# Kernel tuning notes

Measured on AMD Instinct MI355X. Metric: run time of the kernel, lower is better.

Reference implementation:

```python
import jax, jax.numpy as jnp
import numpy as np

N_NODES = 50000
N_EDGES = 800000
IN_CH = 3
HID = 32
OUT_CH = 16
HEADS = 8
NEG_SLOPE = 0.2  # PyG GATConv default LeakyReLU slope


def setup_inputs() -> dict:
    key = jax.random.key(0)
    ks = jax.random.split(key, 12)
    x = jax.random.normal(ks[0], (N_NODES, IN_CH), dtype=jnp.float32)
    edge_index = jax.random.randint(ks[1], (2, N_EDGES), 0, N_NODES, dtype=jnp.int64)
    # Layer 1: GATConv(3 -> 32, heads=8, concat=True)
    s1 = 1.0 / np.sqrt(IN_CH)
    W1 = jax.random.uniform(ks[2], (IN_CH, HEADS * HID), jnp.float32, -s1, s1)
    att_src1 = jax.random.uniform(ks[3], (HEADS, HID), jnp.float32, -s1, s1)
    att_dst1 = jax.random.uniform(ks[4], (HEADS, HID), jnp.float32, -s1, s1)
    bias1 = jnp.zeros((HEADS * HID,), jnp.float32)
    # Layer 2: GATConv(256 -> 16, heads=1, concat=False)
    s2 = 1.0 / np.sqrt(HEADS * HID)
    W2 = jax.random.uniform(ks[5], (HEADS * HID, 1 * OUT_CH), jnp.float32, -s2, s2)
    att_src2 = jax.random.uniform(ks[6], (1, OUT_CH), jnp.float32, -s2, s2)
    att_dst2 = jax.random.uniform(ks[7], (1, OUT_CH), jnp.float32, -s2, s2)
    bias2 = jnp.zeros((OUT_CH,), jnp.float32)
    return {"x": x, "edge_index": edge_index,
            "W1": W1, "att_src1": att_src1, "att_dst1": att_dst1, "bias1": bias1,
            "W2": W2, "att_src2": att_src2, "att_dst2": att_dst2, "bias2": bias2}


def gat_conv(x, src, dst, W, att_src, att_dst, bias, heads, out_ch, concat):
    """PyG-style GATConv (eval mode: attention dropout is identity).
    src/dst already include self-loops. Returns [N, heads*out_ch] or [N, out_ch]."""
    N = x.shape[0]
    h = (x @ W).reshape(N, heads, out_ch)                      # [N,H,C]
    a_s = jnp.einsum("nhc,hc->nh", h, att_src)                 # [N,H]
    a_d = jnp.einsum("nhc,hc->nh", h, att_dst)                 # [N,H]
    e = jax.nn.leaky_relu(a_s[src] + a_d[dst], NEG_SLOPE)      # [E,H]
    # segment softmax over incoming edges of each dst node
    m = jax.ops.segment_max(e, dst, num_segments=N)            # [N,H]
    e = jnp.exp(e - m[dst])
    denom = jax.ops.segment_sum(e, dst, num_segments=N)        # [N,H]
    alpha = e / (denom[dst] + 1e-16)                           # [E,H]
    msg = h[src] * alpha[:, :, None]                           # [E,H,C]
    out = jax.ops.segment_sum(msg, dst, num_segments=N)        # [N,H,C]
    out = out.reshape(N, heads * out_ch) if concat else out.mean(axis=1)
    return out + bias


def reference(x, edge_index, W1, att_src1, att_dst1, bias1, W2, att_src2, att_dst2, bias2):
    N = x.shape[0]
    loop = jnp.arange(N, dtype=edge_index.dtype)
    src = jnp.concatenate([edge_index[0], loop])  # add self-loops (PyG default)
    dst = jnp.concatenate([edge_index[1], loop])
    h = gat_conv(x, src, dst, W1, att_src1, att_dst1, bias1, HEADS, HID, True)
    h = jax.nn.elu(h)
    out = gat_conv(h, src, dst, W2, att_src2, att_dst2, bias2, 1, OUT_CH, False)
    return out
```

## Files before the change

kernel.cpp:

```cpp
#include <hip/hip_runtime.h>
#include <math.h>

#define N_NODES 50000
#define N_EDGES 800000
#define E_TOT   850000
#define HEADS   8
#define HID     32
#define C1      256
#define OUTC    16
#define NEG     0.2f
#define NBKT    196
#define BCAP    6144
#define EPB     2048
#define NSB     ((E_TOT + EPB - 1) / EPB)

__device__ __forceinline__ float lrelu(float v) { return v > 0.0f ? v : NEG * v; }

__device__ unsigned g_bcnt[256];

__global__ __launch_bounds__(256) void k_setup(
    const float* __restrict__ x, const int* __restrict__ ei,
    const float* __restrict__ W1,
    const float* __restrict__ att_s1, const float* __restrict__ att_d1,
    const float* __restrict__ W2,
    const float* __restrict__ att_s2, const float* __restrict__ att_d2,
    float4* __restrict__ xp, unsigned* __restrict__ ebuf,
    float* __restrict__ As1, float* __restrict__ Ad1,
    float* __restrict__ As2, float* __restrict__ Ad2)
{
    __shared__ unsigned hist[256];
    __shared__ unsigned gpos[256];
    int t = threadIdx.x;
    int blk = blockIdx.x;
    if (blk == 0) {
        if (t < 24) {
            int k = t / 8, h = t % 8;
            float as = 0.0f, ad = 0.0f;
            for (int c = 0; c < HID; c++) {
                float w = W1[k * C1 + h * HID + c];
                as = fmaf(w, att_s1[h * HID + c], as);
                ad = fmaf(w, att_d1[h * HID + c], ad);
            }
            As1[k * 8 + h] = as; Ad1[k * 8 + h] = ad;
        }
        float as2 = 0.0f, ad2 = 0.0f;
        for (int j = 0; j < OUTC; j++) {
            float w = W2[t * OUTC + j];
            as2 = fmaf(w, att_s2[j], as2);
            ad2 = fmaf(w, att_d2[j], ad2);
        }
        As2[t] = as2; Ad2[t] = ad2;
    }
    int nid = blk * 256 + t;
    if (nid < N_NODES)
        xp[nid] = make_float4(x[nid * 3], x[nid * 3 + 1], x[nid * 3 + 2], 1.0f);

    hist[t] = 0;
    __syncthreads();
    unsigned pk[8]; unsigned short rk[8]; unsigned char bk[8];
    int e0 = blk * EPB;
    #pragma unroll
    for (int j = 0; j < 8; j++) {
        int e = e0 + j * 256 + t;
        if (e < E_TOT) {
            int s, d;
            if (e < N_EDGES) { s = ei[e]; d = ei[N_EDGES + e]; }
            else             { s = d = e - N_EDGES; }
            pk[j] = ((unsigned)d << 16) | (unsigned)s;
            int b = d >> 8;
            bk[j] = (unsigned char)b;
            rk[j] = (unsigned short)atomicAdd(&hist[b], 1u);
        } else { pk[j] = 0u; bk[j] = 0; rk[j] = 0; }
    }
    __syncthreads();
    unsigned c = hist[t];
    gpos[t] = c ? atomicAdd(&g_bcnt[t], c) : 0u;
    __syncthreads();
    #pragma unroll
    for (int j = 0; j < 8; j++) {
        int e = e0 + j * 256 + t;
        if (e < E_TOT) {
            unsigned b = bk[j];
            ebuf[b * BCAP + gpos[b] + rk[j]] = pk[j];
        }
    }
}

__global__ __launch_bounds__(256) void k_csr(
    const unsigned* __restrict__ ebuf,
    int* __restrict__ off, unsigned short* __restrict__ csr)
{
    __shared__ unsigned s[256];
    __shared__ unsigned dcnt[256];
    __shared__ unsigned dscan[256];
    int t = threadIdx.x, b = blockIdx.x;
    unsigned cntb = g_bcnt[b];
    s[t] = (t < NBKT) ? g_bcnt[t] : 0u;
    dcnt[t] = 0u;
    __syncthreads();
    for (int o = 1; o < 256; o <<= 1) {
        unsigned v = (t >= o) ? s[t - o] : 0u;
        __syncthreads();
        s[t] += v;
        __syncthreads();
    }
    unsigned base = (b == 0) ? 0u : s[b - 1];
    unsigned ev[24]; unsigned short rk[24];
    #pragma unroll
    for (int j = 0; j < 24; j++) {
        int i = j * 256 + t;
        if (i < (int)cntb) {
            unsigned v = ebuf[b * BCAP + i];
            ev[j] = v;
            rk[j] = (unsigned short)atomicAdd(&dcnt[(v >> 16) & 255u], 1u);
        } else { ev[j] = 0u; rk[j] = 0; }
    }
    __syncthreads();
    dscan[t] = dcnt[t];
    __syncthreads();
    for (int o = 1; o < 256; o <<= 1) {
        unsigned v = (t >= o) ? dscan[t - o] : 0u;
        __syncthreads();
        dscan[t] += v;
        __syncthreads();
    }
    int d = b * 256 + t;
    if (d <= N_NODES) off[d] = (int)(base + dscan[t] - dcnt[t]);
    #pragma unroll
    for (int j = 0; j < 24; j++) {
        int i = j * 256 + t;
        if (i < (int)cntb) {
            unsigned d8 = (ev[j] >> 16) & 255u;
            unsigned pos = base + (dscan[d8] - dcnt[d8]) + rk[j];
            csr[pos] = (unsigned short)(ev[j] & 0xFFFFu);
        }
    }
}

__global__ __launch_bounds__(256) void k_agg1(
    const int* __restrict__ off, const unsigned short* __restrict__ csr,
    const float4* __restrict__ xp,
    const float* __restrict__ As1, const float* __restrict__ Ad1,
    float4* __restrict__ xaccw)
{
    int tid = threadIdx.x;
    if (blockIdx.x == 0) g_bcnt[tid] = 0;
    int h = tid & 7;
    int dst = blockIdx.x * 32 + (tid >> 3);
    if (dst >= N_NODES) return;
    float s0 = As1[h], s1 = As1[8 + h], s2 = As1[16 + h];
    float d0 = Ad1[h], d1 = Ad1[8 + h], d2 = Ad1[16 + h];
    float4 xd = xp[dst];
    float ad = xd.x * d0 + xd.y * d1 + xd.z * d2;
    int beg = off[dst], end = off[dst + 1];
    float a0 = 0.0f, a1 = 0.0f, a2 = 0.0f, a3 = 0.0f;
    int k = beg;
    for (; k + 8 <= end; k += 8) {
        int sm[8]; float4 xv[8];
        #pragma unroll
        for (int j = 0; j < 8; j++) sm[j] = csr[k + j];
        #pragma unroll
        for (int j = 0; j < 8; j++) xv[j] = xp[sm[j]];
        #pragma unroll
        for (int j = 0; j < 8; j++) {
            float as = xv[j].x * s0 + xv[j].y * s1 + xv[j].z * s2;
            float p = __expf(lrelu(as + ad));
            a0 = fmaf(p, xv[j].x, a0);
            a1 = fmaf(p, xv[j].y, a1);
            a2 = fmaf(p, xv[j].z, a2);
            a3 += p;
        }
    }
    if (k < end) {
        int m = end - k;
        int sm[8]; float4 xv[8];
        #pragma unroll
        for (int j = 0; j < 8; j++) { int idx = k + j; sm[j] = csr[idx < end ? idx : k]; }
        #pragma unroll
        for (int j = 0; j < 8; j++) xv[j] = xp[sm[j]];
        #pragma unroll
        for (int j = 0; j < 8; j++) {
            float as = xv[j].x * s0 + xv[j].y * s1 + xv[j].z * s2;
            float p = __expf(lrelu(as + ad));
            p = (j < m) ? p : 0.0f;
            a0 = fmaf(p, xv[j].x, a0);
            a1 = fmaf(p, xv[j].y, a1);
            a2 = fmaf(p, xv[j].z, a2);
            a3 += p;
        }
    }
    xaccw[dst * 8 + h] = make_float4(a0, a1, a2, a3);
}

__global__ __launch_bounds__(256) void k_fin1h2(
    const float4* __restrict__ xaccw, const float* __restrict__ W1,
    const float* __restrict__ b1, const float* __restrict__ W2,
    const float* __restrict__ As2, const float* __restrict__ Ad2,
    float* __restrict__ h2, float* __restrict__ a_s2, float* __restrict__ a_d2)
{
    __shared__ float sW1[3 * C1];
    __shared__ float sAux[3 * C1];
    __shared__ float sW2t[OUTC][260];
    __shared__ float sElu[16][260];
    int t = threadIdx.x;
    for (int i = t; i < 3 * C1; i += 256) sW1[i] = W1[i];
    sAux[t] = b1[t]; sAux[C1 + t] = As2[t]; sAux[2 * C1 + t] = Ad2[t];
    for (int i = t; i < C1 * OUTC; i += 256) {
        int k = i >> 4, j = i & 15;
        sW2t[j][k] = W2[i];
    }
    __syncthreads();
    int n = t >> 4, l = t & 15;
    int node = blockIdx.x * 16 + n;
    float as = 0.0f, ad = 0.0f;
    for (int i = 0; i < 16; i++) {
        int c = l + 16 * i;
        int h = c >> 5;
        float4 xa = xaccw[node * 8 + h];
        float z = (xa.x * sW1[c] + xa.y * sW1[C1 + c] + xa.z * sW1[2 * C1 + c])
                  / (xa.w + 1e-16f) + sAux[c];
        float e = z > 0.0f ? z : expm1f(z);
        sElu[n][c] = e;
        as = fmaf(e, sAux[C1 + c], as);
        ad = fmaf(e, sAux[2 * C1 + c], ad);
    }
    for (int o = 1; o < 16; o <<= 1) {
        as += __shfl_xor(as, o, 64);
        ad += __shfl_xor(ad, o, 64);
    }
    if (l == 0) { a_s2[node] = as; a_d2[node] = ad; }
    __syncthreads();
    const float4* e4 = (const float4*)&sElu[n][0];
    const float4* w4 = (const float4*)&sW2t[l][0];
    float acc = 0.0f;
    #pragma unroll 8
    for (int k = 0; k < 64; k++) {
        float4 a = e4[k], b = w4[k];
        acc = fmaf(a.x, b.x, fmaf(a.y, b.y, fmaf(a.z, b.z, fmaf(a.w, b.w, acc))));
    }
    h2[node * OUTC + l] = acc;
}

__global__ __launch_bounds__(256) void k_agg2(
    const int* __restrict__ off, const unsigned short* __restrict__ csr,
    const float* __restrict__ a_s, const float* __restrict__ a_d,
    const float* __restrict__ h2, const float* __restrict__ bias,
    float* __restrict__ out)
{
    int tid = threadIdx.x;
    int c = tid & 15;
    int dst = blockIdx.x * 16 + (tid >> 4);
    if (dst >= N_NODES) return;
    int beg = off[dst], end = off[dst + 1];
    float ad = a_d[dst];
    float acc = 0.0f, denp = 0.0f;
    int k = beg;
    for (; k + 8 <= end; k += 8) {
        int sm[8]; float p[8];
        #pragma unroll
        for (int j = 0; j < 8; j++) sm[j] = csr[k + j];
        #pragma unroll
        for (int j = 0; j < 8; j++) p[j] = __expf(lrelu(a_s[sm[j]] + ad));
        #pragma unroll
        for (int j = 0; j < 8; j++) {
            denp += p[j];
            acc = fmaf(p[j], h2[sm[j] * OUTC + c], acc);
        }
    }
    if (k < end) {
        int m = end - k;
        int sm[8]; float p[8];
        #pragma unroll
        for (int j = 0; j < 8; j++) { int idx = k + j; sm[j] = csr[idx < end ? idx : k]; }
        #pragma unroll
        for (int j = 0; j < 8; j++) {
            float pj = __expf(lrelu(a_s[sm[j]] + ad));
            p[j] = (j < m) ? pj : 0.0f;
        }
        #pragma unroll
        for (int j = 0; j < 8; j++) {
            denp += p[j];
            acc = fmaf(p[j], h2[sm[j] * OUTC + c], acc);
        }
    }
    out[dst * OUTC + c] = acc / (denp + 1e-16f) + bias[c];
}

extern "C" void kernel_launch(void* const* d_in, const int* in_sizes, int n_in,
                              void* d_out, int out_size, void* d_ws, size_t ws_size,
                              hipStream_t stream)
{
    (void)in_sizes; (void)n_in; (void)out_size; (void)ws_size;
    const float* x    = (const float*)d_in[0];
    const int*   ei   = (const int*)d_in[1];
    const float* W1   = (const float*)d_in[2];
    const float* as1w = (const float*)d_in[3];
    const float* ad1w = (const float*)d_in[4];
    const float* b1   = (const float*)d_in[5];
    const float* W2   = (const float*)d_in[6];
    const float* as2w = (const float*)d_in[7];
    const float* ad2w = (const float*)d_in[8];
    const float* b2   = (const float*)d_in[9];
    float* out = (float*)d_out;

    const long N = N_NODES;
    char* p = (char*)d_ws;
    auto alloc = [&](size_t elems) {
        void* r = p; p += ((elems + 3) & ~(size_t)3) * 4; return r;
    };

    float4*         xp     = (float4*)alloc(N * 4);
    float4*         xaccw  = (float4*)alloc(N * HEADS * 4);
    unsigned*       ebuf   = (unsigned*)alloc((size_t)NBKT * BCAP);
    int*            off    = (int*)alloc(N + 1);
    unsigned short* csr    = (unsigned short*)alloc((E_TOT + 1) / 2);
    float*          As1    = (float*)alloc(32);
    float*          Ad1    = (float*)alloc(32);
    float*          As2    = (float*)alloc(C1);
    float*          Ad2    = (float*)alloc(C1);
    float*          h2v    = (float*)alloc(N * OUTC);
    float*          a_s2   = (float*)alloc(N);
    float*          a_d2   = (float*)alloc(N);

    k_setup<<<NSB, 256, 0, stream>>>(
        x, ei, W1, as1w, ad1w, W2, as2w, ad2w,
        xp, ebuf, As1, Ad1, As2, Ad2);
    k_csr<<<NBKT, 256, 0, stream>>>(ebuf, off, csr);
    k_agg1<<<(int)((N + 31) / 32), 256, 0, stream>>>(off, csr, xp, As1, Ad1, xaccw);
    k_fin1h2<<<(int)(N / 16), 256, 0, stream>>>(xaccw, W1, b1, W2, As2, Ad2, h2v, a_s2, a_d2);
    k_agg2<<<(int)((N + 15) / 16), 256, 0, stream>>>(off, csr, a_s2, a_d2, h2v, b2, out);
}
```

Measured before the change: 165.1 us.

## Pre-gather source features into edge-ordered buffer during CSR build, widen CSR blocks

The CSR build kernel now also gathers each edge's source node features into a new edge-ordered float4 array, written at the same position as the CSR index. The layer-1 aggregation then reads these features contiguously instead of doing an index load followed by a random gather. The CSR kernel also goes from 256 to 512 threads per block. The cost is about 13.6 MB of extra scattered writes and reads of a per-edge feature array, in exchange for removing the dependent index-then-gather chain in the aggregation.

New measurement: 166.1 us. No clear change (+0.6%).

```diff
diff --git a/kernel.cpp b/kernel.cpp
--- a/kernel.cpp
+++ b/kernel.cpp
@@ -86,29 +86,29 @@
     }
 }
 
-__global__ __launch_bounds__(256) void k_csr(
-    const unsigned* __restrict__ ebuf,
-    int* __restrict__ off, unsigned short* __restrict__ csr)
+__global__ __launch_bounds__(512) void k_csr(
+    const unsigned* __restrict__ ebuf, const float4* __restrict__ xp,
+    int* __restrict__ off, unsigned short* __restrict__ csr,
+    float4* __restrict__ xpe)
 {
     __shared__ unsigned s[256];
     __shared__ unsigned dcnt[256];
     __shared__ unsigned dscan[256];
     int t = threadIdx.x, b = blockIdx.x;
     unsigned cntb = g_bcnt[b];
-    s[t] = (t < NBKT) ? g_bcnt[t] : 0u;
-    dcnt[t] = 0u;
+    if (t < 256) { s[t] = (t < NBKT) ? g_bcnt[t] : 0u; dcnt[t] = 0u; }
     __syncthreads();
     for (int o = 1; o < 256; o <<= 1) {
-        unsigned v = (t >= o) ? s[t - o] : 0u;
+        unsigned v = (t < 256 && t >= o) ? s[t - o] : 0u;
         __syncthreads();
-        s[t] += v;
+        if (t < 256) s[t] += v;
         __syncthreads();
     }
     unsigned base = (b == 0) ? 0u : s[b - 1];
-    unsigned ev[24]; unsigned short rk[24];
+    unsigned ev[12]; unsigned short rk[12];
     #pragma unroll
-    for (int j = 0; j < 24; j++) {
-        int i = j * 256 + t;
+    for (int j = 0; j < 12; j++) {
+        int i = j * 512 + t;
         if (i < (int)cntb) {
             unsigned v = ebuf[b * BCAP + i];
             ev[j] = v;
@@ -116,29 +116,33 @@
         } else { ev[j] = 0u; rk[j] = 0; }
     }
     __syncthreads();
-    dscan[t] = dcnt[t];
+    if (t < 256) dscan[t] = dcnt[t];
     __syncthreads();
     for (int o = 1; o < 256; o <<= 1) {
-        unsigned v = (t >= o) ? dscan[t - o] : 0u;
+        unsigned v = (t < 256 && t >= o) ? dscan[t - o] : 0u;
         __syncthreads();
-        dscan[t] += v;
+        if (t < 256) dscan[t] += v;
         __syncthreads();
     }
-    int d = b * 256 + t;
-    if (d <= N_NODES) off[d] = (int)(base + dscan[t] - dcnt[t]);
+    if (t < 256) {
+        int d = b * 256 + t;
+        if (d <= N_NODES) off[d] = (int)(base + dscan[t] - dcnt[t]);
+    }
     #pragma unroll
-    for (int j = 0; j < 24; j++) {
-        int i = j * 256 + t;
+    for (int j = 0; j < 12; j++) {
+        int i = j * 512 + t;
         if (i < (int)cntb) {
             unsigned d8 = (ev[j] >> 16) & 255u;
             unsigned pos = base + (dscan[d8] - dcnt[d8]) + rk[j];
-            csr[pos] = (unsigned short)(ev[j] & 0xFFFFu);
+            unsigned src = ev[j] & 0xFFFFu;
+            csr[pos] = (unsigned short)src;
+            xpe[pos] = xp[src];
         }
     }
 }
 
 __global__ __launch_bounds__(256) void k_agg1(
-    const int* __restrict__ off, const unsigned short* __restrict__ csr,
+    const int* __restrict__ off, const float4* __restrict__ xpe,
     const float4* __restrict__ xp,
     const float* __restrict__ As1, const float* __restrict__ Ad1,
     float4* __restrict__ xaccw)
@@ -156,11 +160,9 @@
     float a0 = 0.0f, a1 = 0.0f, a2 = 0.0f, a3 = 0.0f;
     int k = beg;
     for (; k + 8 <= end; k += 8) {
-        int sm[8]; float4 xv[8];
-        #pragma unroll
-        for (int j = 0; j < 8; j++) sm[j] = csr[k + j];
-        #pragma unroll
-        for (int j = 0; j < 8; j++) xv[j] = xp[sm[j]];
+        float4 xv[8];
+        #pragma unroll
+        for (int j = 0; j < 8; j++) xv[j] = xpe[k + j];
         #pragma unroll
         for (int j = 0; j < 8; j++) {
             float as = xv[j].x * s0 + xv[j].y * s1 + xv[j].z * s2;
@@ -173,11 +175,9 @@
     }
     if (k < end) {
         int m = end - k;
-        int sm[8]; float4 xv[8];
-        #pragma unroll
-        for (int j = 0; j < 8; j++) { int idx = k + j; sm[j] = csr[idx < end ? idx : k]; }
-        #pragma unroll
-        for (int j = 0; j < 8; j++) xv[j] = xp[sm[j]];
+        float4 xv[8];
+        #pragma unroll
+        for (int j = 0; j < 8; j++) xv[j] = xpe[k + (j < m ? j : 0)];
         #pragma unroll
         for (int j = 0; j < 8; j++) {
             float as = xv[j].x * s0 + xv[j].y * s1 + xv[j].z * s2;
@@ -311,6 +311,7 @@
 
     float4*         xp     = (float4*)alloc(N * 4);
     float4*         xaccw  = (float4*)alloc(N * HEADS * 4);
+    float4*         xpe    = (float4*)alloc((size_t)E_TOT * 4);
     unsigned*       ebuf   = (unsigned*)alloc((size_t)NBKT * BCAP);
     int*            off    = (int*)alloc(N + 1);
     unsigned short* csr    = (unsigned short*)alloc((E_TOT + 1) / 2);
@@ -325,8 +326,8 @@
     k_setup<<<NSB, 256, 0, stream>>>(
         x, ei, W1, as1w, ad1w, W2, as2w, ad2w,
         xp, ebuf, As1, Ad1, As2, Ad2);
-    k_csr<<<NBKT, 256, 0, stream>>>(ebuf, off, csr);
-    k_agg1<<<(int)((N + 31) / 32), 256, 0, stream>>>(off, csr, xp, As1, Ad1, xaccw);
+    k_csr<<<NBKT, 512, 0, stream>>>(ebuf, xp, off, csr, xpe);
+    k_agg1<<<(int)((N + 31) / 32), 256, 0, stream>>>(off, xpe, xp, As1, Ad1, xaccw);
     k_fin1h2<<<(int)(N / 16), 256, 0, stream>>>(xaccw, W1, b1, W2, As2, Ad2, h2v, a_s2, a_d2);
     k_agg2<<<(int)((N + 15) / 16), 256, 0, stream>>>(off, csr, a_s2, a_d2, h2v, b2, out);
 }
```
